# Optimization experiments

Measured on AMD Instinct MI355X. Metric: run time of the kernel, lower is better.

The kernel has to match this reference:

```python
import jax, jax.numpy as jnp
import numpy as np

EPS_SUM = 1e-8
EPS_FILL = 1e-4
NORM_THRESH = 0.1
MASK_THRESH = 0.1


def _shift1(x):
    # conv2d with 1x3 filter [1,1,0], padding (0,1): out[i] = x[i-1] + x[i]
    return x + jnp.pad(x, ((0, 0), (0, 0), (0, 0), (1, 0)))[..., :-1]


def _shift2(x):
    # conv2d with 1x3 filter [0,1,1], padding (0,1): out[i] = x[i] + x[i+1]
    return x + jnp.pad(x, ((0, 0), (0, 0), (0, 0), (0, 1)))[..., 1:]


def _fill(disp, vm, shift_fn, n_steps):
    # Hole filling: each step propagates valid disparity one pixel; after W
    # steps the data-dependent while-loop of the original has converged
    # (further steps are identity), so a fixed-length scan is equivalent.
    def step(carry, _):
        d, m = carry
        m1 = shift_fn(m)
        nm = (m1 > 0).astype(d.dtype)
        d = d * m + shift_fn(d) / (m1 + EPS_FILL) * (nm - m)
        return (d, nm), None
    (disp, vm), _ = jax.lax.scan(step, (disp, vm), None, length=n_steps)
    return disp, vm


def regress_disp(att, valid_mask):
    # att: [B,H,W,W], valid_mask: [B,1,H,W]
    b, h, w, _ = att.shape
    idx = jnp.arange(w, dtype=att.dtype)
    disp_ini = idx[None, None, None, :] - jnp.sum(att * idx, axis=-1).reshape(b, 1, h, w)
    disp = disp_ini * valid_mask
    disp, vm = _fill(disp, valid_mask, _shift1, w)  # left-to-right pass
    disp, vm = _fill(disp, vm, _shift2, w)          # right-to-left pass
    return disp_ini * valid_mask + disp * (1.0 - valid_mask)


def masked_exp_norm(cost, lower):
    # tril/triu-masked exp normalization (non-standard attention)
    tri = jnp.tril if lower else jnp.triu
    c = tri(cost)
    c = jnp.exp(c - jnp.max(c, axis=-1, keepdims=True))
    c = tri(c)
    return c / (jnp.sum(c, axis=-1, keepdims=True) + EPS_SUM)


def gen_pos_shift(w, dtype):
    p = jnp.linspace(0.0, 2.0, w).astype(dtype)
    pos = jnp.maximum(p[:, None] - p[None, :], 0.0)  # pos_l - pos_r, clipped
    return pos[None, None]  # [1,1,W,W]


def gen_raw_disp(att, pos_shift):
    hi = jnp.argmax(att, axis=-1)
    rr = jnp.stack([hi - 1, hi, hi + 1], axis=-1) + 1  # indices into padded axis
    att_pad = jnp.pad(att, ((0, 0), (0, 0), (0, 0), (1, 1)))
    aw = jnp.take_along_axis(att_pad, rr, axis=-1)
    norm = jnp.sum(aw, axis=-1, keepdims=True)
    norm = jnp.where(norm < NORM_THRESH, 1.0, norm)
    aw = aw / norm
    pos_pad = jnp.broadcast_to(jnp.pad(pos_shift, ((0, 0), (0, 0), (0, 0), (1, 1))), att_pad.shape)
    pr = jnp.take_along_axis(pos_pad, rr, axis=-1)
    return jnp.sum(aw * pr, axis=-1)  # [B,H,W]


def setup_inputs() -> dict:
    key = jax.random.key(0)
    k1, k2 = jax.random.split(key)
    B, H, W = 1, 64, 512
    cost1 = jax.random.normal(k1, (B, H, W, W), dtype=jnp.float32)
    cost2 = jax.random.normal(k2, (B, H, W, W), dtype=jnp.float32)
    return {"cost1": cost1, "cost2": cost2}


def reference(cost1, cost2):
    b, h, w, _ = cost1.shape
    att_r2l = masked_exp_norm(cost2, lower=True)   # right-to-left attention
    att_l2r = masked_exp_norm(cost1, lower=False)  # left-to-right attention
    vm_left = (jnp.sum(att_l2r, axis=-2) > MASK_THRESH).astype(cost1.dtype).reshape(b, 1, h, w)
    vm_right = (jnp.sum(att_r2l, axis=-2) > MASK_THRESH).astype(cost1.dtype).reshape(b, 1, h, w)
    disp_r2l = regress_disp(att_r2l, vm_left)   # [B,1,H,W]
    disp_l2r = regress_disp(att_l2r, vm_right)  # [B,1,H,W]
    pos = gen_pos_shift(w, cost1.dtype)
    raw_l2r = gen_raw_disp(att_r2l, pos)                               # [B,H,W]
    raw_r2l = gen_raw_disp(att_l2r, jnp.swapaxes(pos, -1, -2))         # [B,H,W]
    return jnp.concatenate([disp_r2l, disp_l2r, raw_l2r[:, None], raw_r2l[:, None]], axis=1)
```

## Files before the change

### kernel.cpp

```cpp
#include <hip/hip_runtime.h>
#include <float.h>

#define H 64
#define W 512
#define SPLIT 8


template<bool LOWER>
__device__ __forceinline__ void emit_row(
    const int h, const int p_i, const int p_bj,
    const float p_best, const float p_inv, const float p_wsum,
    const float p_cm, const float p_cp,
    float* __restrict__ disp, float* __restrict__ raw)
{
  const float pscale = 2.0f / 511.0f;
  const int bjm = p_bj - 1, bjp = p_bj + 1;
  const bool pv = LOWER ? (bjm >= 0)   : (bjm >= p_i);
  const bool nv = LOWER ? (bjp <= p_i) : (bjp <= W - 1);
  const float e_h = __expf(p_best);
  const float e_p = pv ? __expf(p_cm) : 0.f;
  const float e_n = nv ? __expf(p_cp) : 0.f;
  const float t0 = e_p + e_h + e_n;
  const float w0 = fmaf(e_p, (float)bjm, fmaf(e_h, (float)p_bj, e_n * (float)bjp));
  const float fi = (float)p_i;
  disp[h * W + p_i] = fi - p_wsum * p_inv;
  const float n0 = t0 * p_inv;
  const float t1 = pscale * (LOWER ? (fi * t0 - w0) : (w0 - fi * t0));
  raw[h * W + p_i] = (t1 * p_inv) / (n0 < 0.1f ? 1.f : n0);
}

template<bool LOWER, bool FULLROW>
__device__ __forceinline__ void process_rows(
    const float* __restrict__ hb, const int h, const int s,
    const int lane, const int wid,
    float* __restrict__ disp, float* __restrict__ raw, float* scol)
{
  constexpr int NH = FULLROW ? 2 : 1;
  constexpr int JB = FULLROW ? 0 : (LOWER ? 0 : 256);

  float cacc[NH * 4];
  #pragma unroll
  for (int q = 0; q < NH * 4; q++) cacc[q] = 0.f;

  int   jmap[NH * 4];
  float jfmap[NH * 4];
  #pragma unroll
  for (int hh = 0; hh < NH; hh++)
    #pragma unroll
    for (int k = 0; k < 4; k++) {
      jmap[hh * 4 + k]  = JB + hh * 256 + lane * 4 + k;
      jfmap[hh * 4 + k] = (float)jmap[hh * 4 + k];
    }

  float c[NH * 4];
  {
    const float* rp0 = hb + (size_t)(s * 64 + wid) * W;
    #pragma unroll
    for (int hh = 0; hh < NH; hh++) {
      const float4 v = ((const float4*)rp0)[(JB >> 2) + hh * 64 + lane];
      c[hh*4+0] = v.x; c[hh*4+1] = v.y; c[hh*4+2] = v.z; c[hh*4+3] = v.w;
    }
  }

  int   p_i = 0, p_bj = 0;
  float p_best = 0.f, p_inv = 0.f, p_wsum = 0.f, p_cm = 0.f, p_cp = 0.f;

  for (int it = 0; it < 8; ++it) {
    const int i = s * 64 + wid + it * 8;
    const float* rp = hb + (size_t)i * W;

    float nc[NH * 4];
    if (it < 7) {
      const float* rn = rp + (size_t)(8 * W);
      #pragma unroll
      for (int hh = 0; hh < NH; hh++) {
        const float4 v = ((const float4*)rn)[(JB >> 2) + hh * 64 + lane];
        nc[hh*4+0] = v.x; nc[hh*4+1] = v.y; nc[hh*4+2] = v.z; nc[hh*4+3] = v.w;
      }
    }

    float best = -FLT_MAX;
    int   bj   = 1024;
    #pragma unroll
    for (int hh = 0; hh < NH; hh++) {
      const bool NM = FULLROW ? (LOWER ? (hh == 1) : (hh == 0)) : true;
      #pragma unroll
      for (int k = 0; k < 4; k++) {
        const int q = hh * 4 + k;
        float v = c[q];
        if (NM) {
          const bool vld = LOWER ? (jmap[q] <= i) : (jmap[q] >= i);
          v = vld ? v : -FLT_MAX;
          c[q] = v;
        }
        if (v > best) { best = v; bj = jmap[q]; }
      }
    }

    float ssum = 0.f, wsum = 0.f;
    #pragma unroll
    for (int q = 0; q < NH * 4; q++) {
      const float e = __expf(c[q]);
      c[q] = e;
      ssum += e;
      wsum = fmaf(e, jfmap[q], wsum);
    }

    #pragma unroll
    for (int off = 32; off; off >>= 1) {
      const float ovb = __shfl_xor(best, off);
      const int   ojb = __shfl_xor(bj, off);
      const float oss = __shfl_xor(ssum, off);
      const float ows = __shfl_xor(wsum, off);
      if (ovb > best || (ovb == best && ojb < bj)) { best = ovb; bj = ojb; }
      ssum += oss;
      wsum += ows;
    }
    const float inv = 1.f / (ssum + 1e-8f);

    const int bjm = bj - 1, bjp = bj + 1;
    const float cm_ = rp[min(max(bjm, 0), W - 1)];
    const float cp_ = rp[min(bjp, W - 1)];

    #pragma unroll
    for (int q = 0; q < NH * 4; q++) cacc[q] = fmaf(c[q], inv, cacc[q]);

    if (it != 0 && lane == 0)
      emit_row<LOWER>(h, p_i, p_bj, p_best, p_inv, p_wsum, p_cm, p_cp,
                      disp, raw);

    p_i = i; p_bj = bj; p_best = best; p_inv = inv; p_wsum = wsum;
    p_cm = cm_; p_cp = cp_;
    if (it < 7) {
      #pragma unroll
      for (int q = 0; q < NH * 4; q++) c[q] = nc[q];
    }
  }
  if (lane == 0)
    emit_row<LOWER>(h, p_i, p_bj, p_best, p_inv, p_wsum, p_cm, p_cp,
                    disp, raw);

  #pragma unroll
  for (int q = 0; q < NH * 4; q++) atomicAdd(&scol[jmap[q]], cacc[q]);
}

__global__ __launch_bounds__(512) void attn_stats_all(
    const float* __restrict__ cost1, const float* __restrict__ cost2,
    float* __restrict__ disp_r2l, float* __restrict__ disp_l2r,
    float* __restrict__ cs_r2l,  float* __restrict__ cs_l2r,
    float* __restrict__ out)
{
  __shared__ float scol[W];
  const int tid  = threadIdx.x;
  const int lane = tid & 63;
  const int wid  = tid >> 6;
  const int gid  = blockIdx.x;
  const bool lower = (gid & 1) == 0;
  const int rest = gid >> 1;
  const int h    = rest >> 3;
  const int s    = rest & 7;

  const float* cost = lower ? cost2 : cost1;
  float* disp = lower ? disp_r2l : disp_l2r;
  float* csum = lower ? cs_r2l  : cs_l2r;
  float* raw  = out + (lower ? 2 : 3) * (H * W);
  const float* hb = cost + (size_t)h * W * W;

  scol[tid] = 0.f;
  __syncthreads();

  if (lower) {
    if (s < 4) process_rows<true,  false>(hb, h, s, lane, wid, disp, raw, scol);
    else       process_rows<true,  true >(hb, h, s, lane, wid, disp, raw, scol);
  } else {
    if (s < 4) process_rows<false, true >(hb, h, s, lane, wid, disp, raw, scol);
    else       process_rows<false, false>(hb, h, s, lane, wid, disp, raw, scol);
  }
  __syncthreads();

  const bool doMine = lower ? (s >= 4 || tid < 256)
                            : (s < 4  || tid >= 256);
  if (doMine) atomicAdd(&csum[h * W + tid], scol[tid]);
}

__global__ __launch_bounds__(64) void fill_rows(
    const float* __restrict__ dispA, const float* __restrict__ csA,
    const float* __restrict__ dispB, const float* __restrict__ csB,
    float* __restrict__ out)
{
  __shared__ float xrow[W];
  const int pair = blockIdx.x >> 6;
  const int h    = blockIdx.x & 63;
  const float* dsp = (pair ? dispB : dispA) + h * W;
  const float* cs  = (pair ? csB  : csA ) + h * W;
  float* o = out + pair * (H * W) + h * W;
  const int lane = threadIdx.x;
  const int j0 = lane * 8;

  float x[8];
  bool m[8];
  int incl[8];
  int run = -1, fv = W;
  #pragma unroll
  for (int k = 0; k < 8; k++) {
    x[k] = dsp[j0 + k];
    m[k] = cs[j0 + k] > 0.1f;
    xrow[j0 + k] = x[k];
    if (m[k]) { run = j0 + k; if (fv == W) fv = j0 + k; }
    incl[k] = run;
  }
  int v = run;
  #pragma unroll
  for (int off = 1; off < 64; off <<= 1) {
    const int tv = __shfl_up(v, off);
    if (lane >= off) v = max(v, tv);
  }
  int excl = __shfl_up(v, 1);
  if (lane == 0) excl = -1;
  int p0 = fv;
  #pragma unroll
  for (int off = 32; off; off >>= 1) p0 = min(p0, __shfl_xor(p0, off));
  __syncthreads();

  const float C2 = -1.4426229e-4f;
  #pragma unroll
  for (int k = 0; k < 8; k++) {
    const int jj = j0 + k;
    float ov;
    if (m[k]) {
      ov = x[k];
    } else {
      const int p = max(excl, incl[k]);
      if (p >= 0)        ov = xrow[p]  * exp2f(C2 * (float)(jj - p));
      else if (p0 < W)   ov = xrow[p0] * exp2f(C2 * (float)(p0 - jj));
      else               ov = 0.f;
    }
    o[jj] = ov;
  }
}

extern "C" void kernel_launch(void* const* d_in, const int* in_sizes, int n_in,
                              void* d_out, int out_size, void* d_ws, size_t ws_size,
                              hipStream_t stream) {
  const float* cost1 = (const float*)d_in[0];
  const float* cost2 = (const float*)d_in[1];
  float* out = (float*)d_out;
  float* w = (float*)d_ws;
  float* disp_r2l_ini = w;
  float* disp_l2r_ini = w + 32768;
  float* cs_l2r       = w + 65536;
  float* cs_r2l       = w + 98304;

  hipMemsetAsync(cs_l2r, 0, 2 * (size_t)H * W * sizeof(float), stream);

  attn_stats_all<<<2 * H * SPLIT, 512, 0, stream>>>(
      cost1, cost2, disp_r2l_ini, disp_l2r_ini, cs_r2l, cs_l2r, out);

  fill_rows<<<2 * H, 64, 0, stream>>>(disp_r2l_ini, cs_l2r,
                                      disp_l2r_ini, cs_r2l, out);
}
```

Before: 161.7 us.

## Fuse hole-filling into stats kernel via per-row completion ticket

Removes the separate fill_rows launch. Each block takes a per-row atomic ticket after publishing its column sums, and the last of the 16 blocks for a row runs the fill for both directions using shared memory. This saves a kernel launch and the inter-kernel gap, at the cost of extra fences and an atomic counter that shares the existing memset. Inside fill_one, __syncthreads is replaced with a block-scope fence, which is safe only because each fill runs within a single wavefront.

```diff
diff --git a/kernel.cpp b/kernel.cpp
--- a/kernel.cpp
+++ b/kernel.cpp
@@ -144,59 +144,11 @@
   for (int q = 0; q < NH * 4; q++) atomicAdd(&scol[jmap[q]], cacc[q]);
 }
 
-__global__ __launch_bounds__(512) void attn_stats_all(
-    const float* __restrict__ cost1, const float* __restrict__ cost2,
-    float* __restrict__ disp_r2l, float* __restrict__ disp_l2r,
-    float* __restrict__ cs_r2l,  float* __restrict__ cs_l2r,
-    float* __restrict__ out)
-{
-  __shared__ float scol[W];
-  const int tid  = threadIdx.x;
-  const int lane = tid & 63;
-  const int wid  = tid >> 6;
-  const int gid  = blockIdx.x;
-  const bool lower = (gid & 1) == 0;
-  const int rest = gid >> 1;
-  const int h    = rest >> 3;
-  const int s    = rest & 7;
-
-  const float* cost = lower ? cost2 : cost1;
-  float* disp = lower ? disp_r2l : disp_l2r;
-  float* csum = lower ? cs_r2l  : cs_l2r;
-  float* raw  = out + (lower ? 2 : 3) * (H * W);
-  const float* hb = cost + (size_t)h * W * W;
-
-  scol[tid] = 0.f;
-  __syncthreads();
-
-  if (lower) {
-    if (s < 4) process_rows<true,  false>(hb, h, s, lane, wid, disp, raw, scol);
-    else       process_rows<true,  true >(hb, h, s, lane, wid, disp, raw, scol);
-  } else {
-    if (s < 4) process_rows<false, true >(hb, h, s, lane, wid, disp, raw, scol);
-    else       process_rows<false, false>(hb, h, s, lane, wid, disp, raw, scol);
-  }
-  __syncthreads();
-
-  const bool doMine = lower ? (s >= 4 || tid < 256)
-                            : (s < 4  || tid >= 256);
-  if (doMine) atomicAdd(&csum[h * W + tid], scol[tid]);
-}
-
-__global__ __launch_bounds__(64) void fill_rows(
-    const float* __restrict__ dispA, const float* __restrict__ csA,
-    const float* __restrict__ dispB, const float* __restrict__ csB,
-    float* __restrict__ out)
-{
-  __shared__ float xrow[W];
-  const int pair = blockIdx.x >> 6;
-  const int h    = blockIdx.x & 63;
-  const float* dsp = (pair ? dispB : dispA) + h * W;
-  const float* cs  = (pair ? csB  : csA ) + h * W;
-  float* o = out + pair * (H * W) + h * W;
-  const int lane = threadIdx.x;
+__device__ __forceinline__ void fill_one(
+    const float* __restrict__ dsp, const float* __restrict__ cs,
+    float* __restrict__ o, const int lane, float* __restrict__ xrow)
+{
   const int j0 = lane * 8;
-
   float x[8];
   bool m[8];
   int incl[8];
@@ -220,7 +172,7 @@
   int p0 = fv;
   #pragma unroll
   for (int off = 32; off; off >>= 1) p0 = min(p0, __shfl_xor(p0, off));
-  __syncthreads();
+  __threadfence_block();
 
   const float C2 = -1.4426229e-4f;
   #pragma unroll
@@ -237,6 +189,62 @@
     }
     o[jj] = ov;
   }
+}
+
+__global__ __launch_bounds__(512) void attn_fused(
+    const float* __restrict__ cost1, const float* __restrict__ cost2,
+    float* __restrict__ disp_r2l, float* __restrict__ disp_l2r,
+    float* __restrict__ cs_r2l,  float* __restrict__ cs_l2r,
+    int* __restrict__ cnt, float* __restrict__ out)
+{
+  __shared__ float scol[W];
+  __shared__ float xrow1[W];
+  __shared__ int sticket;
+  const int tid  = threadIdx.x;
+  const int lane = tid & 63;
+  const int wid  = tid >> 6;
+  const int gid  = blockIdx.x;
+  const bool lower = (gid & 1) == 0;
+  const int rest = gid >> 1;
+  const int h    = rest >> 3;
+  const int s    = rest & 7;
+
+  const float* cost = lower ? cost2 : cost1;
+  float* disp = lower ? disp_r2l : disp_l2r;
+  float* csum = lower ? cs_r2l  : cs_l2r;
+  float* raw  = out + (lower ? 2 : 3) * (H * W);
+  const float* hb = cost + (size_t)h * W * W;
+
+  scol[tid] = 0.f;
+  __syncthreads();
+
+  if (lower) {
+    if (s < 4) process_rows<true,  false>(hb, h, s, lane, wid, disp, raw, scol);
+    else       process_rows<true,  true >(hb, h, s, lane, wid, disp, raw, scol);
+  } else {
+    if (s < 4) process_rows<false, true >(hb, h, s, lane, wid, disp, raw, scol);
+    else       process_rows<false, false>(hb, h, s, lane, wid, disp, raw, scol);
+  }
+  __syncthreads();
+
+  const bool doMine = lower ? (s >= 4 || tid < 256)
+                            : (s < 4  || tid >= 256);
+  if (doMine) atomicAdd(&csum[h * W + tid], scol[tid]);
+
+  __threadfence();
+  __syncthreads();
+  if (tid == 0) sticket = atomicAdd(&cnt[h], 1);
+  __syncthreads();
+  if (sticket != 15) return;
+
+  __threadfence();
+  __syncthreads();
+  if (wid == 0)
+    fill_one(disp_r2l + h * W, cs_l2r + h * W, out + 0 * (H * W) + h * W,
+             lane, scol);
+  else if (wid == 1)
+    fill_one(disp_l2r + h * W, cs_r2l + h * W, out + 1 * (H * W) + h * W,
+             lane, xrow1);
 }
 
 extern "C" void kernel_launch(void* const* d_in, const int* in_sizes, int n_in,
@@ -250,12 +258,10 @@
   float* disp_l2r_ini = w + 32768;
   float* cs_l2r       = w + 65536;
   float* cs_r2l       = w + 98304;
-
-  hipMemsetAsync(cs_l2r, 0, 2 * (size_t)H * W * sizeof(float), stream);
-
-  attn_stats_all<<<2 * H * SPLIT, 512, 0, stream>>>(
-      cost1, cost2, disp_r2l_ini, disp_l2r_ini, cs_r2l, cs_l2r, out);
-
-  fill_rows<<<2 * H, 64, 0, stream>>>(disp_r2l_ini, cs_l2r,
-                                      disp_l2r_ini, cs_r2l, out);
-}
+  int*   cnt          = (int*)(w + 131072);
+
+  hipMemsetAsync(cs_l2r, 0, (2 * (size_t)H * W + H) * sizeof(float), stream);
+
+  attn_fused<<<2 * H * SPLIT, 512, 0, stream>>>(
+      cost1, cost2, disp_r2l_ini, disp_l2r_ini, cs_r2l, cs_l2r, cnt, out);
+}
```

After: 440.9 us. 2.73x slower.
